# Kernel optimization log

Hardware: AMD Instinct MI355X
Metric: run time of the kernel (lower is better)

Reference implementation:

```python
import jax, jax.numpy as jnp
import numpy as np

H = 128
M = 50000
L = 400000
EPS = 1e-9


def setup_inputs() -> dict:
    key = jax.random.key(0)
    ks = jax.random.split(key, 24)
    d = {
        'x_emb': jax.random.normal(ks[0], (M, H), jnp.float32),
        'child_h': jax.random.normal(ks[1], (M, H), jnp.float32),
        'child_c': jax.random.normal(ks[2], (M, H), jnp.float32),
        'pair_cand_idx': jax.random.randint(ks[3], (L,), 0, M, jnp.int32),
        'pair_child_idx': jax.random.randint(ks[4], (L,), 0, M, jnp.int32),
    }
    s = 1.0 / np.sqrt(H)
    names = ['Wi_w', 'Ui_w', 'Wf_w', 'Uf_w', 'Wo_w', 'Uo_w', 'Wc_w', 'Uc_w', 'Wa_w', 'Ua_w']
    for i, n in enumerate(names):
        d[n] = jax.random.uniform(ks[5 + i], (H, H), jnp.float32, -s, s)
    for i, n in enumerate(['Wi_b', 'Wf_b', 'Wo_b', 'Wc_b', 'Wa_b']):
        d[n] = jax.random.uniform(ks[15 + i], (H,), jnp.float32, -s, s)
    d['v_w'] = jax.random.uniform(ks[20], (H,), jnp.float32, -s, s)
    return d


def reference(x_emb, child_h, child_c, pair_cand_idx, pair_child_idx,
              Wi_w, Ui_w, Wf_w, Uf_w, Wo_w, Uo_w, Wc_w, Uc_w, Wa_w, Ua_w,
              Wi_b, Wf_b, Wo_b, Wc_b, Wa_b, v_w):
    m = x_emb.shape[0]
    ci, chi = pair_cand_idx, pair_child_idx

    # --- segment attention (torch version runs under no_grad) ---
    Ah = child_h @ Wa_w.T + Wa_b          # [M,H]
    Bx = x_emb @ Ua_w.T                   # [M,H]
    e = jnp.tanh(Ah[chi] + Bx[ci]) @ v_w  # [L]
    seg_max = jax.ops.segment_max(e, ci, num_segments=m)
    x_exp = jnp.exp(e - seg_max[ci])
    seg_sum = jax.ops.segment_sum(x_exp, ci, num_segments=m) + EPS
    attn = x_exp / seg_sum[ci]            # [L]
    h_hat = jax.ops.segment_sum(attn[:, None] * child_h[chi], ci, num_segments=m)  # [M,H]

    # --- tree-LSTM gates ---
    i_j = jax.nn.sigmoid(x_emb @ Wi_w.T + Wi_b + h_hat @ Ui_w.T)
    Wfx = x_emb @ Wf_w.T + Wf_b
    Ufh = child_h @ Uf_w.T
    f_pair = jax.nn.sigmoid(Wfx[ci] + Ufh[chi])                       # [L,H]
    sum_f_c = jax.ops.segment_sum(f_pair * child_c[chi], ci, num_segments=m)
    c_t = jnp.tanh(x_emb @ Wc_w.T + Wc_b + h_hat @ Uc_w.T)
    c = i_j * c_t + sum_f_c
    o_j = jax.nn.sigmoid(x_emb @ Wo_w.T + Wo_b + h_hat @ Uo_w.T)
    h = o_j * jnp.tanh(c)
    return (h, c)
```

## Files before the change

### kernel.cpp

```cpp
#include <hip/hip_runtime.h>
#include <cstdint>
#include <cstddef>

#define H 128
#define PSTRIDE 512

typedef __bf16 v8bf __attribute__((ext_vector_type(8)));
typedef __bf16 v4bf __attribute__((ext_vector_type(4)));
typedef float  v4f  __attribute__((ext_vector_type(4)));

__device__ __forceinline__ float ftanh(float x) {
    return 1.f - 2.f / (1.f + __expf(2.f * x));
}
__device__ __forceinline__ float fsigm(float x) {
    return 1.f / (1.f + __expf(-x));
}

__device__ __forceinline__ float red32(float s) {
    int x;
    x = __builtin_amdgcn_update_dpp(0, __float_as_int(s), 0xB1, 0xF, 0xF, true);
    s += __int_as_float(x);
    x = __builtin_amdgcn_update_dpp(0, __float_as_int(s), 0x4E, 0xF, 0xF, true);
    s += __int_as_float(x);
    x = __builtin_amdgcn_update_dpp(0, __float_as_int(s), 0x141, 0xF, 0xF, true);
    s += __int_as_float(x);
    x = __builtin_amdgcn_update_dpp(0, __float_as_int(s), 0x140, 0xF, 0xF, true);
    s += __int_as_float(x);
    x = __builtin_amdgcn_ds_swizzle(__float_as_int(s), 0x401F);
    return s + __int_as_float(x);
}

struct MatDesc {
    const __bf16* A;
    int           lda;
    const __bf16* Wb;
    const float*  bias;
    __bf16*       C;
    int           ldc;
    int           psec;
};
struct MatBatch { MatDesc m[7]; };
struct WPtrs { const float* w[10]; };

__global__ __launch_bounds__(256) void prep_k(WPtrs wp, __bf16* __restrict__ Wb,
                                              const float* __restrict__ x,
                                              const float* __restrict__ chh,
                                              const float* __restrict__ chc,
                                              __bf16* __restrict__ xe,
                                              __bf16* __restrict__ chA,
                                              __bf16* __restrict__ P,
                                              const int* __restrict__ ci,
                                              int* __restrict__ counts,
                                              int MH4, int L) {
    int tid = blockIdx.x * 256 + threadIdx.x;
    if (tid < 40960) {
        int mat = tid >> 12;
        int off = (tid & 4095) << 2;
        v4f a = *(const v4f*)(wp.w[mat] + off);
        v4bf b;
#pragma unroll
        for (int k = 0; k < 4; ++k) b[k] = (__bf16)a[k];
        *(v4bf*)(Wb + mat * 16384 + off) = b;
        return;
    }
    int i = tid - 40960;
    if (i < MH4) {
        v4f a = ((const v4f*)x)[i];
        v4f b = ((const v4f*)chh)[i];
        v4f c = ((const v4f*)chc)[i];
        v4bf ab, bb, cb;
#pragma unroll
        for (int k = 0; k < 4; ++k) {
            ab[k] = (__bf16)a[k]; bb[k] = (__bf16)b[k]; cb[k] = (__bf16)c[k];
        }
        ((v4bf*)xe)[i] = ab;
        ((v4bf*)chA)[i] = bb;
        int m = i >> 5;
        int q = i & 31;
        __bf16* prow = P + (size_t)m * PSTRIDE + (q << 4);
        *(v4bf*)prow = bb;
        *(v4bf*)(prow + 4) = cb;
        return;
    }
    int l = i - MH4;
    if (l < L) atomicAdd(&counts[ci[l]], 1);
}

__global__ __launch_bounds__(256) void gemm_batch(MatBatch batch, int M, int ntile) {
    const int blk = blockIdx.x;
    const int g = blk / 56;
    const int w = blk % 56;
    const int j = w >> 3;
    const int t = (g << 3) | (w & 7);
    if (t >= ntile) return;
    const MatDesc d = batch.m[j];
    __shared__ __bf16 wlds[H][H + 8];

    for (int tt = threadIdx.x; tt < 2048; tt += 256) {
        int n = tt >> 4;
        int k = (tt & 15) << 3;
        *(v8bf*)&wlds[n][k] = *(const v8bf*)(d.Wb + n * H + k);
    }
    __syncthreads();

    const int wave = threadIdx.x >> 6;
    const int lane = threadIdx.x & 63;
    const int quad = lane >> 4;
    const int l16  = lane & 15;
    const int r0   = t * 128 + wave * 32;

    int ra = r0 + l16;      if (ra > M - 1) ra = M - 1;
    int rb = r0 + 16 + l16; if (rb > M - 1) rb = M - 1;

    const __bf16* p0 = d.A + (size_t)ra * d.lda + quad * 8;
    const __bf16* p1 = d.A + (size_t)rb * d.lda + quad * 8;
    v8bf a0[4], a1[4];
#pragma unroll
    for (int k0 = 0; k0 < 4; ++k0) {
        a0[k0] = *(const v8bf*)(p0 + k0 * 32);
        a1[k0] = *(const v8bf*)(p1 + k0 * 32);
    }

    v4f acc0[8], acc1[8];
#pragma unroll
    for (int nt = 0; nt < 8; ++nt) {
        acc0[nt] = (v4f){0.f, 0.f, 0.f, 0.f};
        acc1[nt] = (v4f){0.f, 0.f, 0.f, 0.f};
    }

#pragma unroll
    for (int k0 = 0; k0 < 4; ++k0) {
#pragma unroll
        for (int nt = 0; nt < 8; ++nt) {
            v8bf b = *(const v8bf*)(&wlds[nt * 16 + l16][k0 * 32 + quad * 8]);
            acc0[nt] = __builtin_amdgcn_mfma_f32_16x16x32_bf16(a0[k0], b, acc0[nt], 0, 0, 0);
            acc1[nt] = __builtin_amdgcn_mfma_f32_16x16x32_bf16(a1[k0], b, acc1[nt], 0, 0, 0);
        }
    }

    if (d.psec >= 0) {
        const int so = d.psec << 2;
#pragma unroll
        for (int nt = 0; nt < 8; ++nt) {
            int n = nt * 16 + l16;
            float bia = d.bias ? d.bias[n] : 0.f;
            size_t col = ((size_t)(n >> 2) << 4) + so + (n & 3);
#pragma unroll
            for (int r = 0; r < 4; ++r) {
                int m0 = r0 + quad * 4 + r;
                int m1 = m0 + 16;
                if (m0 < M) d.C[(size_t)m0 * PSTRIDE + col] = (__bf16)(acc0[nt][r] + bia);
                if (m1 < M) d.C[(size_t)m1 * PSTRIDE + col] = (__bf16)(acc1[nt][r] + bia);
            }
        }
    } else {
#pragma unroll
        for (int nt = 0; nt < 8; ++nt) {
            int n = nt * 16 + l16;
            float bia = d.bias ? d.bias[n] : 0.f;
#pragma unroll
            for (int r = 0; r < 4; ++r) {
                int m0 = r0 + quad * 4 + r;
                int m1 = m0 + 16;
                if (m0 < M) d.C[(size_t)m0 * d.ldc + n] = (__bf16)(acc0[nt][r] + bia);
                if (m1 < M) d.C[(size_t)m1 * d.ldc + n] = (__bf16)(acc1[nt][r] + bia);
            }
        }
    }
}

__global__ __launch_bounds__(1024) void scan_local(const int* __restrict__ counts,
                                                   int* __restrict__ excl,
                                                   int* __restrict__ bsums, int M) {
    __shared__ int s[1024];
    int tid = threadIdx.x;
    int idx = blockIdx.x * 1024 + tid;
    int v = (idx < M) ? counts[idx] : 0;
    s[tid] = v;
    __syncthreads();
    for (int off = 1; off < 1024; off <<= 1) {
        int t = (tid >= off) ? s[tid - off] : 0;
        __syncthreads();
        s[tid] += t;
        __syncthreads();
    }
    if (idx < M) excl[idx] = s[tid] - v;
    if (tid == 1023) bsums[blockIdx.x] = s[1023];
}

__global__ __launch_bounds__(1024) void scan_fused(int* __restrict__ rowptr,
                                                   int* __restrict__ cursor,
                                                   const int* __restrict__ bsums,
                                                   const int* __restrict__ counts,
                                                   int M, int nb) {
    __shared__ int s[1024];
    int t = threadIdx.x, b = blockIdx.x;
    int v = (t < nb) ? bsums[t] : 0;
    s[t] = v;
    __syncthreads();
    for (int off = 1; off < 1024; off <<= 1) {
        int tt = (t >= off) ? s[t - off] : 0;
        __syncthreads();
        s[t] += tt;
        __syncthreads();
    }
    int boff = (b == 0) ? 0 : s[b - 1];
    int idx = b * 1024 + t;
    if (idx < M) {
        int val = rowptr[idx] + boff;
        rowptr[idx] = val;
        cursor[idx] = val;
        if (idx == M - 1) rowptr[M] = val + counts[M - 1];
    }
}

__global__ __launch_bounds__(256) void scatter_k(const int* __restrict__ ci,
                                                 const int* __restrict__ chi,
                                                 int* __restrict__ cursor,
                                                 int* __restrict__ payload, int L) {
    int l = blockIdx.x * 256 + threadIdx.x;
    if (l < L) {
        int pos = atomicAdd(&cursor[ci[l]], 1);
        payload[pos] = chi[l];
    }
}

__global__ __launch_bounds__(128) void segment_fused(const int* __restrict__ rowptr,
                                                     const int* __restrict__ payload,
                                                     const float* __restrict__ vw,
                                                     const __bf16* __restrict__ Bx,
                                                     const __bf16* __restrict__ Wfx,
                                                     const __bf16* __restrict__ P,
                                                     __bf16* __restrict__ hhat,
                                                     float* __restrict__ sumfc, int M) {
    const int wl   = threadIdx.x & 63;
    const int half = wl & 32;
    const int l32  = wl & 31;
    const int m = blockIdx.x * 4 + (threadIdx.x >> 5);
    if (m >= M) return;
    const int start = rowptr[m];
    const int deg   = rowptr[m + 1] - start;
    const int h   = l32 << 2;
    const int q16 = l32 << 4;

    v4bf bx4 = *(const v4bf*)(Bx + (m << 7) + h);
    v4bf wf4 = *(const v4bf*)(Wfx + (m << 7) + h);
    v4f  vv  = *(const v4f*)(vw + h);
    float bxf[4], wff[4];
#pragma unroll
    for (int k = 0; k < 4; ++k) { bxf[k] = (float)bx4[k]; wff[k] = (float)wf4[k]; }

    int pl0 = (l32 < deg) ? payload[start + l32] : 0;
    int pl1 = (32 + l32 < deg) ? payload[start + 32 + l32] : 0;

    float denom = 0.f;
    float acch[4] = {0.f, 0.f, 0.f, 0.f};
    float accf[4] = {0.f, 0.f, 0.f, 0.f};

    const int jcap = deg < 64 ? deg : 64;
    for (int j = 0; j < jcap; ++j) {
        int cj = __shfl((j & 32) ? pl1 : pl0, half | (j & 31), 64);
        const __bf16* pb = P + ((size_t)cj << 9) + q16;
        v8bf x0 = *(const v8bf*)pb;
        v8bf x1 = *(const v8bf*)(pb + 8);
        float s = 0.f;
#pragma unroll
        for (int k = 0; k < 4; ++k) s += ftanh((float)x1[4 + k] + bxf[k]) * vv[k];
        s = red32(s);
        float ex = __expf(s);
        denom += ex;
#pragma unroll
        for (int k = 0; k < 4; ++k) {
            acch[k] = fmaf(ex, (float)x0[k], acch[k]);
            accf[k] += fsigm(wff[k] + (float)x1[k]) * (float)x0[4 + k];
        }
    }
    for (int j = 64; j < deg; ++j) {
        int cj = payload[start + j];
        const __bf16* pb = P + ((size_t)cj << 9) + q16;
        v8bf x0 = *(const v8bf*)pb;
        v8bf x1 = *(const v8bf*)(pb + 8);
        float s = 0.f;
#pragma unroll
        for (int k = 0; k < 4; ++k) s += ftanh((float)x1[4 + k] + bxf[k]) * vv[k];
        s = red32(s);
        float ex = __expf(s);
        denom += ex;
#pragma unroll
        for (int k = 0; k < 4; ++k) {
            acch[k] = fmaf(ex, (float)x0[k], acch[k]);
            accf[k] += fsigm(wff[k] + (float)x1[k]) * (float)x0[4 + k];
        }
    }

    float inv = 1.f / (denom + 1e-9f);
    v4bf hb;
    v4f sf;
#pragma unroll
    for (int k = 0; k < 4; ++k) { hb[k] = (__bf16)(acch[k] * inv); sf[k] = accf[k]; }
    *(v4bf*)(hhat + (size_t)m * H + h) = hb;
    *(v4f*)(sumfc + (size_t)m * H + h) = sf;
}

__global__ __launch_bounds__(256) void gemm_final(const __bf16* __restrict__ hhat,
                                                  const __bf16* __restrict__ Ui,
                                                  const __bf16* __restrict__ Uc,
                                                  const __bf16* __restrict__ Uo,
                                                  const __bf16* __restrict__ Xi,
                                                  const __bf16* __restrict__ Xc,
                                                  const __bf16* __restrict__ Xo,
                                                  const float* __restrict__ sumfc,
                                                  float* __restrict__ out, int M, int MH) {
    const int wave = threadIdx.x >> 6;
    const int lane = threadIdx.x & 63;
    const int quad = lane >> 4;
    const int l16  = lane & 15;
    const int r0   = blockIdx.x * 128 + wave * 32;
    const int nt0  = blockIdx.y * 2;

    const __bf16* p0 = hhat + (size_t)(r0 + l16) * H + quad * 8;
    const __bf16* p1 = hhat + (size_t)(r0 + 16 + l16) * H + quad * 8;
    v8bf a0[4], a1[4];
#pragma unroll
    for (int k0 = 0; k0 < 4; ++k0) {
        a0[k0] = *(const v8bf*)(p0 + k0 * 32);
        a1[k0] = *(const v8bf*)(p1 + k0 * 32);
    }

#pragma unroll
    for (int ntl = 0; ntl < 2; ++ntl) {
        const int nt = nt0 + ntl;
        const int boff = (nt * 16 + l16) * H + quad * 8;
        v4f ai0 = (v4f){0.f, 0.f, 0.f, 0.f}, ai1 = ai0;
        v4f ac0 = ai0, ac1 = ai0, ao0 = ai0, ao1 = ai0;
#pragma unroll
        for (int k0 = 0; k0 < 4; ++k0) {
            v8bf bi = *(const v8bf*)(Ui + boff + k0 * 32);
            v8bf bc = *(const v8bf*)(Uc + boff + k0 * 32);
            v8bf bo = *(const v8bf*)(Uo + boff + k0 * 32);
            ai0 = __builtin_amdgcn_mfma_f32_16x16x32_bf16(a0[k0], bi, ai0, 0, 0, 0);
            ai1 = __builtin_amdgcn_mfma_f32_16x16x32_bf16(a1[k0], bi, ai1, 0, 0, 0);
            ac0 = __builtin_amdgcn_mfma_f32_16x16x32_bf16(a0[k0], bc, ac0, 0, 0, 0);
            ac1 = __builtin_amdgcn_mfma_f32_16x16x32_bf16(a1[k0], bc, ac1, 0, 0, 0);
            ao0 = __builtin_amdgcn_mfma_f32_16x16x32_bf16(a0[k0], bo, ao0, 0, 0, 0);
            ao1 = __builtin_amdgcn_mfma_f32_16x16x32_bf16(a1[k0], bo, ao1, 0, 0, 0);
        }
        int n = nt * 16 + l16;
#pragma unroll
        for (int r = 0; r < 4; ++r) {
            int m0 = r0 + quad * 4 + r;
            if (m0 < M) {
                size_t idx = (size_t)m0 * H + n;
                float ig = fsigm((float)Xi[idx] + ai0[r]);
                float ct = ftanh((float)Xc[idx] + ac0[r]);
                float og = fsigm((float)Xo[idx] + ao0[r]);
                float c = ig * ct + sumfc[idx];
                out[idx] = og * ftanh(c);
                out[MH + idx] = c;
            }
            int m1 = m0 + 16;
            if (m1 < M) {
                size_t idx = (size_t)m1 * H + n;
                float ig = fsigm((float)Xi[idx] + ai1[r]);
                float ct = ftanh((float)Xc[idx] + ac1[r]);
                float og = fsigm((float)Xo[idx] + ao1[r]);
                float c = ig * ct + sumfc[idx];
                out[idx] = og * ftanh(c);
                out[MH + idx] = c;
            }
        }
    }
}

extern "C" void kernel_launch(void* const* d_in, const int* in_sizes, int n_in,
                              void* d_out, int out_size, void* d_ws, size_t ws_size,
                              hipStream_t stream) {
    const float* x_emb   = (const float*)d_in[0];
    const float* child_h = (const float*)d_in[1];
    const float* child_c = (const float*)d_in[2];
    const int*   ci      = (const int*)d_in[3];
    const int*   chi     = (const int*)d_in[4];
    const float* Wi_b = (const float*)d_in[15];
    const float* Wf_b = (const float*)d_in[16];
    const float* Wo_b = (const float*)d_in[17];
    const float* Wc_b = (const float*)d_in[18];
    const float* Wa_b = (const float*)d_in[19];
    const float* vw   = (const float*)d_in[20];

    const int M    = in_sizes[0] / H;
    const int L    = in_sizes[3];
    const int Mpad = (M + 127) & ~127;
    const int MH   = M * H;
    const int MH4  = MH / 4;

    char* p = (char*)d_ws;
    auto alloc = [&](size_t bytes) {
        char* r = p;
        p += (bytes + 255) & ~(size_t)255;
        return (void*)r;
    };
    size_t bfbytes = (size_t)Mpad * H * sizeof(__bf16);
    __bf16* xe16   = (__bf16*)alloc(bfbytes);
    __bf16* chA16  = (__bf16*)alloc(bfbytes);
    __bf16* P      = (__bf16*)alloc((size_t)Mpad * PSTRIDE * sizeof(__bf16));
    __bf16* hhat16 = (__bf16*)alloc(bfbytes);
    __bf16* Bx16   = (__bf16*)alloc(bfbytes);
    __bf16* Wfx16  = (__bf16*)alloc(bfbytes);
    __bf16* Xi16   = (__bf16*)alloc(bfbytes);
    __bf16* Xc16   = (__bf16*)alloc(bfbytes);
    __bf16* Xo16   = (__bf16*)alloc(bfbytes);
    __bf16* Wb     = (__bf16*)alloc(10 * 16384 * sizeof(__bf16));
    float* sumfc   = (float*)alloc((size_t)MH * 4);
    int*   payload = (int*)alloc((size_t)L * 4);
    int*   counts  = (int*)alloc((size_t)M * 4);
    int*   rowptr  = (int*)alloc((size_t)(M + 1) * 4);
    int*   cursor  = (int*)alloc((size_t)M * 4);
    int*   bsums   = (int*)alloc(1024 * 4);

    hipMemsetAsync(counts, 0, (size_t)M * 4, stream);

    WPtrs wp;
    for (int k = 0; k < 10; ++k) wp.w[k] = (const float*)d_in[5 + k];
    int prep_items = 40960 + MH4 + L;
    prep_k<<<(prep_items + 255) / 256, 256, 0, stream>>>(wp, Wb, x_emb, child_h, child_c,
                                                         xe16, chA16, P, ci, counts, MH4, L);

    const __bf16* Wi = Wb + 0 * 16384;
    const __bf16* Ui = Wb + 1 * 16384;
    const __bf16* Wf = Wb + 2 * 16384;
    const __bf16* Uf = Wb + 3 * 16384;
    const __bf16* Wo = Wb + 4 * 16384;
    const __bf16* Uo = Wb + 5 * 16384;
    const __bf16* Wc = Wb + 6 * 16384;
    const __bf16* Uc = Wb + 7 * 16384;
    const __bf16* Wa = Wb + 8 * 16384;
    const __bf16* Ua = Wb + 9 * 16384;

    MatBatch ba{};
    ba.m[0] = MatDesc{chA16, H, Wa, Wa_b,    P,     0, 3};
    ba.m[1] = MatDesc{xe16,  H, Ua, nullptr, Bx16,  H, -1};
    ba.m[2] = MatDesc{xe16,  H, Wf, Wf_b,    Wfx16, H, -1};
    ba.m[3] = MatDesc{chA16, H, Uf, nullptr, P,     0, 2};
    ba.m[4] = MatDesc{xe16,  H, Wi, Wi_b,    Xi16,  H, -1};
    ba.m[5] = MatDesc{xe16,  H, Wc, Wc_b,    Xc16,  H, -1};
    ba.m[6] = MatDesc{xe16,  H, Wo, Wo_b,    Xo16,  H, -1};
    const int ntile = Mpad / 128;
    const int ntile8 = (ntile + 7) & ~7;
    gemm_batch<<<7 * ntile8, 256, 0, stream>>>(ba, M, ntile);

    int nb = (M + 1023) / 1024;
    scan_local<<<nb, 1024, 0, stream>>>(counts, rowptr, bsums, M);
    scan_fused<<<nb, 1024, 0, stream>>>(rowptr, cursor, bsums, counts, M, nb);

    scatter_k<<<(L + 255) / 256, 256, 0, stream>>>(ci, chi, cursor, payload, L);

    segment_fused<<<(M + 3) / 4, 128, 0, stream>>>(rowptr, payload, vw, Bx16, Wfx16, P,
                                                   hhat16, sumfc, M);

    gemm_final<<<dim3(Mpad / 128, 4), 256, 0, stream>>>(hhat16, Ui, Uc, Uo, Xi16, Xc16, Xo16,
                                                        sumfc, (float*)d_out, M, MH);
}
```

Measured before the change: 408.9 us.

## Fuse child-side GEMMs into a pair kernel writing the packed buffer, prefetch gathers

Adds a pair_k kernel that reads child_h in fp32, converts it in registers, and computes both the Wa and Uf projections in one pass. It stages the results in LDS and writes fully packed 16-element rows of P (h, c, Uf, Wa) with vector stores. This replaces the scattered 2-byte strided P writes and the separate bf16 child_h copy, and cuts gemm_batch from 7 matrices to 5. The segment loop also prefetches the next gathered P row before computing the current one to hide gather latency, at the cost of extra registers and one more launch.

```diff
diff --git a/kernel.cpp b/kernel.cpp
--- a/kernel.cpp
+++ b/kernel.cpp
@@ -37,18 +37,13 @@
     const float*  bias;
     __bf16*       C;
     int           ldc;
-    int           psec;
 };
-struct MatBatch { MatDesc m[7]; };
+struct MatBatch { MatDesc m[5]; };
 struct WPtrs { const float* w[10]; };
 
 __global__ __launch_bounds__(256) void prep_k(WPtrs wp, __bf16* __restrict__ Wb,
                                               const float* __restrict__ x,
-                                              const float* __restrict__ chh,
-                                              const float* __restrict__ chc,
                                               __bf16* __restrict__ xe,
-                                              __bf16* __restrict__ chA,
-                                              __bf16* __restrict__ P,
                                               const int* __restrict__ ci,
                                               int* __restrict__ counts,
                                               int MH4, int L) {
@@ -66,30 +61,132 @@
     int i = tid - 40960;
     if (i < MH4) {
         v4f a = ((const v4f*)x)[i];
-        v4f b = ((const v4f*)chh)[i];
-        v4f c = ((const v4f*)chc)[i];
-        v4bf ab, bb, cb;
-#pragma unroll
-        for (int k = 0; k < 4; ++k) {
-            ab[k] = (__bf16)a[k]; bb[k] = (__bf16)b[k]; cb[k] = (__bf16)c[k];
-        }
+        v4bf ab;
+#pragma unroll
+        for (int k = 0; k < 4; ++k) ab[k] = (__bf16)a[k];
         ((v4bf*)xe)[i] = ab;
-        ((v4bf*)chA)[i] = bb;
-        int m = i >> 5;
-        int q = i & 31;
-        __bf16* prow = P + (size_t)m * PSTRIDE + (q << 4);
-        *(v4bf*)prow = bb;
-        *(v4bf*)(prow + 4) = cb;
         return;
     }
     int l = i - MH4;
     if (l < L) atomicAdd(&counts[ci[l]], 1);
 }
 
+__global__ __launch_bounds__(256) void pair_k(const float* __restrict__ chh,
+                                              const float* __restrict__ chc,
+                                              const __bf16* __restrict__ Wa,
+                                              const __bf16* __restrict__ Uf,
+                                              const float* __restrict__ bia,
+                                              __bf16* __restrict__ P,
+                                              int M, int ntile) {
+    const int blk = blockIdx.x;
+    const int w16 = blk % 16;
+    const int t   = (blk / 16) * 8 + (w16 & 7);
+    const int nh  = w16 >> 3;
+    if (t >= ntile) return;
+
+    __shared__ __bf16 lds[2][64][136];
+
+    for (int tt = threadIdx.x; tt < 2048; tt += 256) {
+        int ws = tt >> 10;
+        int ln = (tt >> 4) & 63;
+        int k  = (tt & 15) << 3;
+        const __bf16* src = ws ? Uf : Wa;
+        *(v8bf*)&lds[ws][ln][k] = *(const v8bf*)(src + (nh * 64 + ln) * H + k);
+    }
+    __syncthreads();
+
+    const int wave = threadIdx.x >> 6;
+    const int lane = threadIdx.x & 63;
+    const int quad = lane >> 4;
+    const int l16  = lane & 15;
+    const int r0   = t * 128 + wave * 32;
+
+    int ra = r0 + l16;      if (ra > M - 1) ra = M - 1;
+    int rb = r0 + 16 + l16; if (rb > M - 1) rb = M - 1;
+
+    const float* p0 = chh + (size_t)ra * H + quad * 8;
+    const float* p1 = chh + (size_t)rb * H + quad * 8;
+    v8bf a0[4], a1[4];
+#pragma unroll
+    for (int k0 = 0; k0 < 4; ++k0) {
+        v4f x0a = *(const v4f*)(p0 + k0 * 32);
+        v4f x0b = *(const v4f*)(p0 + k0 * 32 + 4);
+        v4f x1a = *(const v4f*)(p1 + k0 * 32);
+        v4f x1b = *(const v4f*)(p1 + k0 * 32 + 4);
+        v8bf t0, t1;
+#pragma unroll
+        for (int k = 0; k < 4; ++k) {
+            t0[k] = (__bf16)x0a[k]; t0[k + 4] = (__bf16)x0b[k];
+            t1[k] = (__bf16)x1a[k]; t1[k + 4] = (__bf16)x1b[k];
+        }
+        a0[k0] = t0; a1[k0] = t1;
+    }
+
+    v4f acc[2][4][2];
+#pragma unroll
+    for (int ws = 0; ws < 2; ++ws)
+#pragma unroll
+        for (int ntl = 0; ntl < 4; ++ntl)
+#pragma unroll
+            for (int rg = 0; rg < 2; ++rg) acc[ws][ntl][rg] = (v4f){0.f, 0.f, 0.f, 0.f};
+
+#pragma unroll
+    for (int k0 = 0; k0 < 4; ++k0) {
+#pragma unroll
+        for (int ntl = 0; ntl < 4; ++ntl) {
+            v8bf bwa = *(const v8bf*)(&lds[0][ntl * 16 + l16][k0 * 32 + quad * 8]);
+            v8bf buf = *(const v8bf*)(&lds[1][ntl * 16 + l16][k0 * 32 + quad * 8]);
+            acc[0][ntl][0] = __builtin_amdgcn_mfma_f32_16x16x32_bf16(a0[k0], bwa, acc[0][ntl][0], 0, 0, 0);
+            acc[0][ntl][1] = __builtin_amdgcn_mfma_f32_16x16x32_bf16(a1[k0], bwa, acc[0][ntl][1], 0, 0, 0);
+            acc[1][ntl][0] = __builtin_amdgcn_mfma_f32_16x16x32_bf16(a0[k0], buf, acc[1][ntl][0], 0, 0, 0);
+            acc[1][ntl][1] = __builtin_amdgcn_mfma_f32_16x16x32_bf16(a1[k0], buf, acc[1][ntl][1], 0, 0, 0);
+        }
+    }
+    __syncthreads();
+
+    __bf16 (*stg)[128][68] = reinterpret_cast<__bf16 (*)[128][68]>(&lds[0][0][0]);
+#pragma unroll
+    for (int ws = 0; ws < 2; ++ws)
+#pragma unroll
+        for (int ntl = 0; ntl < 4; ++ntl) {
+            int lcol = ntl * 16 + l16;
+            float bv = (ws == 0) ? bia[nh * 64 + lcol] : 0.f;
+#pragma unroll
+            for (int rg = 0; rg < 2; ++rg)
+#pragma unroll
+                for (int r = 0; r < 4; ++r) {
+                    int lrow = wave * 32 + rg * 16 + quad * 4 + r;
+                    stg[ws][lrow][lcol] = (__bf16)(acc[ws][ntl][rg][r] + bv);
+                }
+        }
+    __syncthreads();
+
+    for (int id = threadIdx.x; id < 2048; id += 256) {
+        int lrow = id >> 4;
+        int lq   = id & 15;
+        int m = t * 128 + lrow;
+        if (m >= M) continue;
+        int q = nh * 16 + lq;
+        v4f hv = *(const v4f*)(chh + (size_t)m * H + q * 4);
+        v4f cv = *(const v4f*)(chc + (size_t)m * H + q * 4);
+        v8bf o0, o1;
+#pragma unroll
+        for (int kk = 0; kk < 4; ++kk) {
+            o0[kk]     = (__bf16)hv[kk];
+            o0[4 + kk] = (__bf16)cv[kk];
+            o1[kk]     = stg[1][lrow][lq * 4 + kk];
+            o1[4 + kk] = stg[0][lrow][lq * 4 + kk];
+        }
+        __bf16* dst = P + (size_t)m * PSTRIDE + ((size_t)q << 4);
+        *(v8bf*)dst = o0;
+        *(v8bf*)(dst + 8) = o1;
+    }
+}
+
 __global__ __launch_bounds__(256) void gemm_batch(MatBatch batch, int M, int ntile) {
     const int blk = blockIdx.x;
-    const int g = blk / 56;
-    const int w = blk % 56;
+    const int g = blk / 40;
+    const int w = blk % 40;
     const int j = w >> 3;
     const int t = (g << 3) | (w & 7);
     if (t >= ntile) return;
@@ -138,33 +235,16 @@
         }
     }
 
-    if (d.psec >= 0) {
-        const int so = d.psec << 2;
-#pragma unroll
-        for (int nt = 0; nt < 8; ++nt) {
-            int n = nt * 16 + l16;
-            float bia = d.bias ? d.bias[n] : 0.f;
-            size_t col = ((size_t)(n >> 2) << 4) + so + (n & 3);
-#pragma unroll
-            for (int r = 0; r < 4; ++r) {
-                int m0 = r0 + quad * 4 + r;
-                int m1 = m0 + 16;
-                if (m0 < M) d.C[(size_t)m0 * PSTRIDE + col] = (__bf16)(acc0[nt][r] + bia);
-                if (m1 < M) d.C[(size_t)m1 * PSTRIDE + col] = (__bf16)(acc1[nt][r] + bia);
-            }
-        }
-    } else {
-#pragma unroll
-        for (int nt = 0; nt < 8; ++nt) {
-            int n = nt * 16 + l16;
-            float bia = d.bias ? d.bias[n] : 0.f;
-#pragma unroll
-            for (int r = 0; r < 4; ++r) {
-                int m0 = r0 + quad * 4 + r;
-                int m1 = m0 + 16;
-                if (m0 < M) d.C[(size_t)m0 * d.ldc + n] = (__bf16)(acc0[nt][r] + bia);
-                if (m1 < M) d.C[(size_t)m1 * d.ldc + n] = (__bf16)(acc1[nt][r] + bia);
-            }
+#pragma unroll
+    for (int nt = 0; nt < 8; ++nt) {
+        int n = nt * 16 + l16;
+        float bia = d.bias ? d.bias[n] : 0.f;
+#pragma unroll
+        for (int r = 0; r < 4; ++r) {
+            int m0 = r0 + quad * 4 + r;
+            int m1 = m0 + 16;
+            if (m0 < M) d.C[(size_t)m0 * d.ldc + n] = (__bf16)(acc0[nt][r] + bia);
+            if (m1 < M) d.C[(size_t)m1 * d.ldc + n] = (__bf16)(acc1[nt][r] + bia);
         }
     }
 }
@@ -258,21 +338,31 @@
     float accf[4] = {0.f, 0.f, 0.f, 0.f};
 
     const int jcap = deg < 64 ? deg : 64;
-    for (int j = 0; j < jcap; ++j) {
-        int cj = __shfl((j & 32) ? pl1 : pl0, half | (j & 31), 64);
-        const __bf16* pb = P + ((size_t)cj << 9) + q16;
-        v8bf x0 = *(const v8bf*)pb;
-        v8bf x1 = *(const v8bf*)(pb + 8);
-        float s = 0.f;
-#pragma unroll
-        for (int k = 0; k < 4; ++k) s += ftanh((float)x1[4 + k] + bxf[k]) * vv[k];
-        s = red32(s);
-        float ex = __expf(s);
-        denom += ex;
-#pragma unroll
-        for (int k = 0; k < 4; ++k) {
-            acch[k] = fmaf(ex, (float)x0[k], acch[k]);
-            accf[k] += fsigm(wff[k] + (float)x1[k]) * (float)x0[4 + k];
+    if (jcap > 0) {
+        int cj0 = __shfl(pl0, half, 64);
+        const __bf16* pb0 = P + ((size_t)cj0 << 9) + q16;
+        v8bf x0 = *(const v8bf*)pb0;
+        v8bf x1 = *(const v8bf*)(pb0 + 8);
+        for (int j = 0; j < jcap; ++j) {
+            v8bf y0 = x0, y1 = x1;
+            int jn = j + 1;
+            if (jn < jcap) {
+                int cjn = __shfl((jn & 32) ? pl1 : pl0, half | (jn & 31), 64);
+                const __bf16* pbn = P + ((size_t)cjn << 9) + q16;
+                x0 = *(const v8bf*)pbn;
+                x1 = *(const v8bf*)(pbn + 8);
+            }
+            float s = 0.f;
+#pragma unroll
+            for (int k = 0; k < 4; ++k) s += ftanh((float)y1[4 + k] + bxf[k]) * vv[k];
+            s = red32(s);
+            float ex = __expf(s);
+            denom += ex;
+#pragma unroll
+            for (int k = 0; k < 4; ++k) {
+                acch[k] = fmaf(ex, (float)y0[k], acch[k]);
+                accf[k] += fsigm(wff[k] + (float)y1[k]) * (float)y0[4 + k];
+            }
         }
     }
     for (int j = 64; j < deg; ++j) {
@@ -401,7 +491,6 @@
     };
     size_t bfbytes = (size_t)Mpad * H * sizeof(__bf16);
     __bf16* xe16   = (__bf16*)alloc(bfbytes);
-    __bf16* chA16  = (__bf16*)alloc(bfbytes);
     __bf16* P      = (__bf16*)alloc((size_t)Mpad * PSTRIDE * sizeof(__bf16));
     __bf16* hhat16 = (__bf16*)alloc(bfbytes);
     __bf16* Bx16   = (__bf16*)alloc(bfbytes);
@@ -422,8 +511,8 @@
     WPtrs wp;
     for (int k = 0; k < 10; ++k) wp.w[k] = (const float*)d_in[5 + k];
     int prep_items = 40960 + MH4 + L;
-    prep_k<<<(prep_items + 255) / 256, 256, 0, stream>>>(wp, Wb, x_emb, child_h, child_c,
-                                                         xe16, chA16, P, ci, counts, MH4, L);
+    prep_k<<<(prep_items + 255) / 256, 256, 0, stream>>>(wp, Wb, x_emb, xe16,
+                                                         ci, counts, MH4, L);
 
     const __bf16* Wi = Wb + 0 * 16384;
     const __bf16* Ui = Wb + 1 * 16384;
@@ -436,17 +525,18 @@
     const __bf16* Wa = Wb + 8 * 16384;
     const __bf16* Ua = Wb + 9 * 16384;
 
-    MatBatch ba{};
-    ba.m[0] = MatDesc{chA16, H, Wa, Wa_b,    P,     0, 3};
-    ba.m[1] = MatDesc{xe16,  H, Ua, nullptr, Bx16,  H, -1};
-    ba.m[2] = MatDesc{xe16,  H, Wf, Wf_b,    Wfx16, H, -1};
-    ba.m[3] = MatDesc{chA16, H, Uf, nullptr, P,     0, 2};
-    ba.m[4] = MatDesc{xe16,  H, Wi, Wi_b,    Xi16,  H, -1};
-    ba.m[5] = MatDesc{xe16,  H, Wc, Wc_b,    Xc16,  H, -1};
-    ba.m[6] = MatDesc{xe16,  H, Wo, Wo_b,    Xo16,  H, -1};
     const int ntile = Mpad / 128;
     const int ntile8 = (ntile + 7) & ~7;
-    gemm_batch<<<7 * ntile8, 256, 0, stream>>>(ba, M, ntile);
+
+    pair_k<<<2 * ntile8, 256, 0, stream>>>(child_h, child_c, Wa, Uf, Wa_b, P, M, ntile);
+
+    MatBatch ba{};
+    ba.m[0] = MatDesc{xe16, H, Ua, nullptr, Bx16,  H};
+    ba.m[1] = MatDesc{xe16, H, Wf, Wf_b,    Wfx16, H};
+    ba.m[2] = MatDesc{xe16, H, Wi, Wi_b,    Xi16,  H};
+    ba.m[3] = MatDesc{xe16, H, Wc, Wc_b,    Xc16,  H};
+    ba.m[4] = MatDesc{xe16, H, Wo, Wo_b,    Xo16,  H};
+    gemm_batch<<<5 * ntile8, 256, 0, stream>>>(ba, M, ntile);
 
     int nb = (M + 1023) / 1024;
     scan_local<<<nb, 1024, 0, stream>>>(counts, rowptr, bsums, M);
```

Result: no change. 416.1 us (+1.7%).
